# Kernel tuning notes

Hardware: AMD Instinct MI355X
Metric: run time of the kernel (lower is better)

## Reference

```python
import jax, jax.numpy as jnp
import numpy as np

N_NODES = 100000
N_EDGES = 1600000
D = 128


def setup_inputs() -> dict:
    key = jax.random.key(0)
    k1, k2, k3, k4 = jax.random.split(key, 4)
    x = jax.random.normal(k1, (N_NODES, D), dtype=jnp.float32)
    # scale weights by 1/sqrt(fan_in) (matches typical init, keeps exp(e) stable)
    W = jax.random.normal(k2, (D, D), dtype=jnp.float32) / np.sqrt(D)
    a = jax.random.normal(k3, (2 * D,), dtype=jnp.float32) / np.sqrt(2 * D)
    edge_index = jax.random.randint(k4, (2, N_EDGES), 0, N_NODES, dtype=jnp.int64)
    return {"x": x, "W": W, "a": a, "edge_index": edge_index}


def reference(x, W, a, edge_index):
    # x: [N, in], W: [out, in] (torch Linear layout), a: [2*out], edge_index: [2, E]
    N = x.shape[0]
    d_out = W.shape[0]
    h = x @ W.T                                   # [N, out]
    src = edge_index[0]
    tgt = edge_index[1]
    # a(cat([h_src, h_tgt])) == h_src @ a[:d] + h_tgt @ a[d:] — avoids [E, 2d] concat
    s_src = h @ a[:d_out]                         # [N]
    s_tgt = h @ a[d_out:]                         # [N]
    e = jax.nn.leaky_relu(s_src[src] + s_tgt[tgt], negative_slope=0.2)  # [E]
    att = jnp.exp(e)                              # [E]
    att_sum = jax.ops.segment_sum(att, tgt, num_segments=N)             # [N]
    att_norm = att / (att_sum[tgt] + 1e-8)        # [E] (dropout=0 / eval mode)
    h_prime = jax.ops.segment_sum(h[src] * att_norm[:, None], tgt, num_segments=N)  # [N, out]
    h_prime = h_prime + x                          # residual (in_features == out_features)
    return jax.nn.elu(h_prime)
```

## Files before the change

kernel.cpp:

```cpp
#include <hip/hip_runtime.h>
#include <hip/hip_bf16.h>

#define DD 128
#define CAP 56
#define NBPW 128
#define CHUNK 4096
#define LBIN 832

typedef _Float16 half8  __attribute__((ext_vector_type(8)));
typedef _Float16 half2t __attribute__((ext_vector_type(2)));
typedef float f32x4 __attribute__((ext_vector_type(4)));

__device__ __forceinline__ ushort h16bits(float f) {
    _Float16 h = (_Float16)f;
    return __builtin_bit_cast(ushort, h);
}
__device__ __forceinline__ half8 pack8h(float4 lo, float4 hi) {
    half8 r;
    r[0] = (_Float16)lo.x; r[1] = (_Float16)lo.y;
    r[2] = (_Float16)lo.z; r[3] = (_Float16)lo.w;
    r[4] = (_Float16)hi.x; r[5] = (_Float16)hi.y;
    r[6] = (_Float16)hi.z; r[7] = (_Float16)hi.w;
    return r;
}
__device__ __forceinline__ float fdot2u(uint pair, uint avp, float c) {
    return __builtin_amdgcn_fdot2(__builtin_bit_cast(half2t, pair),
                                  __builtin_bit_cast(half2t, avp), c, false);
}

__global__ __launch_bounds__(256) void prep_w(
    const float* __restrict__ W, _Float16* __restrict__ Wh) {
    int i = blockIdx.x * 256 + threadIdx.x;
    if (i < DD * DD) Wh[i] = (_Float16)W[i];
}

__global__ __launch_bounds__(256, 2) void mfma_gemm_kernel(
    const float* __restrict__ x, const _Float16* __restrict__ Wh,
    const float* __restrict__ a, ushort* __restrict__ h,
    float* __restrict__ ssrc, float* __restrict__ stgt, int N, int nTiles) {
    __shared__ ushort hl[4][16][136];
    const int wid = threadIdx.x >> 6;
    const int l   = threadIdx.x & 63;
    const int lr  = l & 15;
    const int lk  = l >> 4;

    half8 Bf[4][8];
    #pragma unroll
    for (int kt = 0; kt < 4; ++kt)
        #pragma unroll
        for (int n = 0; n < 8; ++n)
            Bf[kt][n] = *(const half8*)(Wh + (size_t)(n * 16 + lr) * DD + kt * 32 + lk * 8);
    float avs[8], avt[8];
    #pragma unroll
    for (int n = 0; n < 8; ++n) {
        avs[n] = a[n * 16 + lr];
        avt[n] = a[DD + n * 16 + lr];
    }

    for (int tile = blockIdx.x; tile < nTiles; tile += gridDim.x) {
        const int rowBase = tile * 64 + wid * 16;
        const int arow = rowBase + lr;
        f32x4 acc[8];
        #pragma unroll
        for (int n = 0; n < 8; ++n) acc[n] = (f32x4){0.f, 0.f, 0.f, 0.f};

        #pragma unroll
        for (int kt = 0; kt < 4; ++kt) {
            float4 x0, x1;
            if (arow < N) {
                const float* xp = x + (size_t)arow * DD + kt * 32 + lk * 8;
                x0 = *(const float4*)xp;
                x1 = *(const float4*)(xp + 4);
            } else {
                x0 = make_float4(0.f, 0.f, 0.f, 0.f);
                x1 = x0;
            }
            half8 A = pack8h(x0, x1);
            #pragma unroll
            for (int n = 0; n < 8; ++n)
                acc[n] = __builtin_amdgcn_mfma_f32_16x16x32_f16(A, Bf[kt][n], acc[n], 0, 0, 0);
        }

        float ps[4] = {0.f, 0.f, 0.f, 0.f}, pt[4] = {0.f, 0.f, 0.f, 0.f};
        #pragma unroll
        for (int n = 0; n < 8; ++n)
            #pragma unroll
            for (int r = 0; r < 4; ++r) {
                ps[r] = fmaf(acc[n][r], avs[n], ps[r]);
                pt[r] = fmaf(acc[n][r], avt[n], pt[r]);
            }
        #pragma unroll
        for (int r = 0; r < 4; ++r) {
            #pragma unroll
            for (int m = 8; m >= 1; m >>= 1) {
                ps[r] += __shfl_xor(ps[r], m);
                pt[r] += __shfl_xor(pt[r], m);
            }
        }
        if (lr == 0) {
            #pragma unroll
            for (int r = 0; r < 4; ++r) {
                int grow = rowBase + lk * 4 + r;
                if (grow < N) { ssrc[grow] = ps[r]; stgt[grow] = pt[r]; }
            }
        }

        __syncthreads();
        #pragma unroll
        for (int n = 0; n < 8; ++n)
            #pragma unroll
            for (int r = 0; r < 4; ++r)
                hl[wid][lk * 4 + r][n * 16 + lr] = h16bits(acc[n][r]);
        __syncthreads();
        if (arow < N) {
            uint4* dst = (uint4*)(h + (size_t)arow * DD + lk * 32);
            const uint4* s4 = (const uint4*)&hl[wid][lr][lk * 32];
            dst[0] = s4[0]; dst[1] = s4[1]; dst[2] = s4[2]; dst[3] = s4[3];
        }
    }
}

__global__ __launch_bounds__(256) void p1_count(
    const int* __restrict__ tgt, int* __restrict__ H, int E, int nbin, int nblk) {
    __shared__ int lh[LBIN];
    const int blk = blockIdx.x;
    for (int i = threadIdx.x; i < nbin; i += 256) lh[i] = 0;
    __syncthreads();
    const int base = blk * CHUNK;
    const int end = min(E, base + CHUNK);
    for (int e = base + threadIdx.x; e < end; e += 256)
        atomicAdd(&lh[tgt[e] >> 7], 1);
    __syncthreads();
    for (int i = threadIdx.x; i < nbin; i += 256) H[i * nblk + blk] = lh[i];
}

__global__ __launch_bounds__(256) void p2a_colscan(
    int* __restrict__ H, int* __restrict__ binTot, int nblk) {
    __shared__ int lds[256];
    const int o = blockIdx.x * nblk;
    const int t = threadIdx.x;
    int a0 = (2 * t     < nblk) ? H[o + 2 * t]     : 0;
    int a1 = (2 * t + 1 < nblk) ? H[o + 2 * t + 1] : 0;
    int s = a0 + a1;
    lds[t] = s;
    __syncthreads();
    int val = s;
    for (int off = 1; off < 256; off <<= 1) {
        int u = (t >= off) ? lds[t - off] : 0;
        __syncthreads();
        val += u;
        lds[t] = val;
        __syncthreads();
    }
    int excl = val - s;
    if (2 * t     < nblk) H[o + 2 * t]     = excl;
    if (2 * t + 1 < nblk) H[o + 2 * t + 1] = excl + a0;
    if (t == 255) binTot[blockIdx.x] = val;
}

__global__ __launch_bounds__(256) void p2b_binscan(
    const int* __restrict__ binTot, int* __restrict__ binOff, int nbin) {
    __shared__ int lds[256];
    const int t = threadIdx.x;
    int v[4];
    int s = 0;
    #pragma unroll
    for (int j = 0; j < 4; ++j) {
        int idx = t * 4 + j;
        v[j] = (idx < nbin) ? binTot[idx] : 0;
        s += v[j];
    }
    lds[t] = s;
    __syncthreads();
    int val = s;
    for (int off = 1; off < 256; off <<= 1) {
        int u = (t >= off) ? lds[t - off] : 0;
        __syncthreads();
        val += u;
        lds[t] = val;
        __syncthreads();
    }
    int excl = val - s;
    #pragma unroll
    for (int j = 0; j < 4; ++j) {
        int idx = t * 4 + j;
        if (idx < nbin) binOff[idx] = excl;
        excl += v[j];
    }
    if (t == 255) binOff[nbin] = val;
}

__global__ __launch_bounds__(256) void p3_partition(
    const int* __restrict__ src, const int* __restrict__ tgt,
    const int* __restrict__ H, const int* __restrict__ binOff,
    uint* __restrict__ ebuf, int E, int nbin, int nblk) {
    __shared__ int lcur[LBIN];
    const int blk = blockIdx.x;
    for (int i = threadIdx.x; i < nbin; i += 256) lcur[i] = 0;
    __syncthreads();
    const int base = blk * CHUNK;
    const int end = min(E, base + CHUNK);
    for (int e = base + threadIdx.x; e < end; e += 256) {
        int s = src[e], t = tgt[e];
        int tb = t >> 7;
        int r = atomicAdd(&lcur[tb], 1);
        int slot = binOff[tb] + H[tb * nblk + blk] + r;
        ebuf[slot] = ((uint)(t & 127) << 17) | (uint)s;
    }
}

__global__ __launch_bounds__(256) void p4_bucket(
    const uint* __restrict__ ebuf, const int* __restrict__ binOff,
    int* __restrict__ srcS, int* __restrict__ deg, int N) {
    __shared__ int cur[NBPW];
    const int bin = blockIdx.x;
    const int n0 = bin * NBPW;
    for (int i = threadIdx.x; i < NBPW; i += 256) cur[i] = 0;
    __syncthreads();
    const int beg = binOff[bin], end = binOff[bin + 1];
    for (int i = beg + threadIdx.x; i < end; i += 256) {
        uint v = ebuf[i];
        int tl = (int)(v >> 17);
        int s  = (int)(v & 0x1FFFFu);
        int pos = atomicAdd(&cur[tl], 1);
        if (pos < CAP) srcS[(size_t)(n0 + tl) * CAP + pos] = s;
    }
    __syncthreads();
    for (int i = threadIdx.x; i < NBPW; i += 256) {
        int node = n0 + i;
        if (node < N) deg[node] = cur[i];
    }
}

__global__ __launch_bounds__(256) void gather_acc_kernel(
    const int* __restrict__ srcS, const int* __restrict__ degA,
    const float* __restrict__ ssrc, const float* __restrict__ stgt,
    const ushort* __restrict__ h, const float* __restrict__ x,
    float* __restrict__ out, int N) {
    const int node = blockIdx.x * 4 + (threadIdx.x >> 6);
    if (node >= N) return;
    const int lane = threadIdx.x & 63;
    const int q = lane >> 4, l4 = lane & 15;

    int deg = degA[node];
    if (deg > CAP) deg = CAP;
    const size_t base = (size_t)node * CAP;

    int   sv = 0;
    float attv = 0.f;
    if (lane < deg) {
        sv = srcS[base + lane];
        float v = ssrc[sv] + stgt[node];
        v = v > 0.f ? v : 0.2f * v;
        attv = __expf(v);
    }
    float asum = attv;
    #pragma unroll
    for (int m = 32; m >= 1; m >>= 1) asum += __shfl_xor(asum, m);
    const float inv = 1.f / (asum + 1e-8f);
    const uint pv = ((uint)h16bits(attv) << 17) | (uint)sv;

    const int passes = (deg + 3) >> 2;
    float acc[8] = {0.f, 0.f, 0.f, 0.f, 0.f, 0.f, 0.f, 0.f};

    #define PAIR_STEP(pv0, pv1)                                                  \
    {                                                                            \
        int s0 = (int)((pv0) & 0x1FFFFu), s1 = (int)((pv1) & 0x1FFFFu);          \
        uint4 hv0 = *(const uint4*)(h + ((size_t)s0 << 7) + (l4 << 3));          \
        uint4 hv1 = *(const uint4*)(h + ((size_t)s1 << 7) + (l4 << 3));          \
        uint avp = ((pv0) >> 17) | (((pv1) >> 17) << 16);                        \
        uint p0, p1;                                                             \
        p0 = __builtin_amdgcn_perm(hv1.x, hv0.x, 0x05040100u);                   \
        p1 = __builtin_amdgcn_perm(hv1.x, hv0.x, 0x07060302u);                   \
        acc[0] = fdot2u(p0, avp, acc[0]); acc[1] = fdot2u(p1, avp, acc[1]);      \
        p0 = __builtin_amdgcn_perm(hv1.y, hv0.y, 0x05040100u);                   \
        p1 = __builtin_amdgcn_perm(hv1.y, hv0.y, 0x07060302u);                   \
        acc[2] = fdot2u(p0, avp, acc[2]); acc[3] = fdot2u(p1, avp, acc[3]);      \
        p0 = __builtin_amdgcn_perm(hv1.z, hv0.z, 0x05040100u);                   \
        p1 = __builtin_amdgcn_perm(hv1.z, hv0.z, 0x07060302u);                   \
        acc[4] = fdot2u(p0, avp, acc[4]); acc[5] = fdot2u(p1, avp, acc[5]);      \
        p0 = __builtin_amdgcn_perm(hv1.w, hv0.w, 0x05040100u);                   \
        p1 = __builtin_amdgcn_perm(hv1.w, hv0.w, 0x07060302u);                   \
        acc[6] = fdot2u(p0, avp, acc[6]); acc[7] = fdot2u(p1, avp, acc[7]);      \
    }

    int p = 0;
    for (; p + 4 <= passes; p += 4) {
        const int i0 = (p << 2) + q;
        uint a0 = (uint)__shfl((int)pv, i0);
        uint a1 = (uint)__shfl((int)pv, i0 + 4);
        uint a2 = (uint)__shfl((int)pv, i0 + 8);
        uint a3 = (uint)__shfl((int)pv, i0 + 12);
        PAIR_STEP(a0, a1);
        PAIR_STEP(a2, a3);
    }
    if (p + 2 <= passes) {
        const int i0 = (p << 2) + q;
        uint a0 = (uint)__shfl((int)pv, i0);
        uint a1 = (uint)__shfl((int)pv, i0 + 4);
        PAIR_STEP(a0, a1);
        p += 2;
    }
    if (p < passes) {
        const int i0 = (p << 2) + q;
        uint a0 = (uint)__shfl((int)pv, i0);
        int s0 = (int)(a0 & 0x1FFFFu);
        uint avp = a0 >> 17;
        uint4 hv0 = *(const uint4*)(h + ((size_t)s0 << 7) + (l4 << 3));
        acc[0] = fdot2u(hv0.x, avp, acc[0]); acc[1] = fdot2u(hv0.x >> 16, avp, acc[1]);
        acc[2] = fdot2u(hv0.y, avp, acc[2]); acc[3] = fdot2u(hv0.y >> 16, avp, acc[3]);
        acc[4] = fdot2u(hv0.z, avp, acc[4]); acc[5] = fdot2u(hv0.z >> 16, avp, acc[5]);
        acc[6] = fdot2u(hv0.w, avp, acc[6]); acc[7] = fdot2u(hv0.w >> 16, avp, acc[7]);
    }
    #undef PAIR_STEP

    #pragma unroll
    for (int j = 0; j < 8; ++j) {
        acc[j] += __shfl_xor(acc[j], 16);
        acc[j] += __shfl_xor(acc[j], 32);
    }

    if (q == 0) {
        const float4* xp = (const float4*)(x + (size_t)node * DD + l4 * 8);
        float4 x0 = xp[0], x1 = xp[1];
        float o[8];
        o[0] = fmaf(acc[0], inv, x0.x); o[1] = fmaf(acc[1], inv, x0.y);
        o[2] = fmaf(acc[2], inv, x0.z); o[3] = fmaf(acc[3], inv, x0.w);
        o[4] = fmaf(acc[4], inv, x1.x); o[5] = fmaf(acc[5], inv, x1.y);
        o[6] = fmaf(acc[6], inv, x1.z); o[7] = fmaf(acc[7], inv, x1.w);
        #pragma unroll
        for (int j = 0; j < 8; ++j) o[j] = o[j] > 0.f ? o[j] : expm1f(o[j]);
        float4* op = (float4*)(out + (size_t)node * DD + l4 * 8);
        op[0] = make_float4(o[0], o[1], o[2], o[3]);
        op[1] = make_float4(o[4], o[5], o[6], o[7]);
    }
}

extern "C" void kernel_launch(void* const* d_in, const int* in_sizes, int n_in,
                              void* d_out, int out_size, void* d_ws, size_t ws_size,
                              hipStream_t stream) {
    const float* x  = (const float*)d_in[0];
    const float* W  = (const float*)d_in[1];
    const float* a  = (const float*)d_in[2];
    const int*   ei = (const int*)d_in[3];

    const int N = in_sizes[0] / DD;
    const int E = in_sizes[3] / 2;
    const int* src = ei;
    const int* tgt = ei + E;

    float* out = (float*)d_out;

    const int nbin = (N + NBPW - 1) / NBPW;
    const int nblk = (E + CHUNK - 1) / CHUNK;

    char* w = (char*)d_ws;
    int*      srcS   = (int*)w;               w += (size_t)N * CAP * 4;
    ushort*   h      = (ushort*)w;            w += (size_t)N * DD * 2;
    float*    ssrc   = (float*)w;             w += (size_t)N * 4;
    float*    stgt   = (float*)w;             w += (size_t)N * 4;
    int*      deg    = (int*)w;               w += (size_t)N * 4;
    uint*     ebuf   = (uint*)w;              w += (size_t)E * 4;
    _Float16* Wh     = (_Float16*)w;          w += (size_t)DD * DD * 2;
    int*      H      = (int*)w;               w += (size_t)nbin * nblk * 4;
    int*      binTot = (int*)w;               w += (size_t)nbin * 4;
    int*      binOff = (int*)w;               w += (size_t)(nbin + 1) * 4;

    const int nTiles = (N + 63) / 64;

    prep_w<<<(DD * DD + 255) / 256, 256, 0, stream>>>(W, Wh);
    mfma_gemm_kernel<<<640, 256, 0, stream>>>(x, Wh, a, h, ssrc, stgt, N, nTiles);

    p1_count<<<nblk, 256, 0, stream>>>(tgt, H, E, nbin, nblk);
    p2a_colscan<<<nbin, 256, 0, stream>>>(H, binTot, nblk);
    p2b_binscan<<<1, 256, 0, stream>>>(binTot, binOff, nbin);
    p3_partition<<<nblk, 256, 0, stream>>>(src, tgt, H, binOff, ebuf, E, nbin, nblk);
    p4_bucket<<<nbin, 256, 0, stream>>>(ebuf, binOff, srcS, deg, N);

    gather_acc_kernel<<<(N + 3) / 4, 256, 0, stream>>>(srcS, deg, ssrc, stgt,
                                                       h, x, out, N);
}
```

Baseline: 164.3 us.

## Fuse histogram into GEMM, inline bin scan, half-wave per node gather

Merges the edge-count histogram into the GEMM kernel, which now launches one block per 64-row tile instead of a persistent grid. The bin-offset scan moves into every partition and bucket block, which removes two launches. The gather kernel now assigns a half-wave to each node, stages the packed (attention, src) pairs in LDS instead of using lane shuffles, and loads x early. The cost is redundant scan work in every block, and high-degree nodes now get fewer lanes each.

```diff
diff --git a/kernel.cpp b/kernel.cpp
--- a/kernel.cpp
+++ b/kernel.cpp
@@ -34,11 +34,14 @@
     if (i < DD * DD) Wh[i] = (_Float16)W[i];
 }
 
-__global__ __launch_bounds__(256, 2) void mfma_gemm_kernel(
+__global__ __launch_bounds__(256, 2) void gemm_hist_kernel(
     const float* __restrict__ x, const _Float16* __restrict__ Wh,
     const float* __restrict__ a, ushort* __restrict__ h,
-    float* __restrict__ ssrc, float* __restrict__ stgt, int N, int nTiles) {
+    float* __restrict__ ssrc, float* __restrict__ stgt,
+    const int* __restrict__ tgt, int* __restrict__ H,
+    int N, int E, int nbin, int nblk) {
     __shared__ ushort hl[4][16][136];
+    __shared__ int lh[LBIN];
     const int wid = threadIdx.x >> 6;
     const int l   = threadIdx.x & 63;
     const int lr  = l & 15;
@@ -57,81 +60,76 @@
         avt[n] = a[DD + n * 16 + lr];
     }
 
-    for (int tile = blockIdx.x; tile < nTiles; tile += gridDim.x) {
-        const int rowBase = tile * 64 + wid * 16;
-        const int arow = rowBase + lr;
-        f32x4 acc[8];
-        #pragma unroll
-        for (int n = 0; n < 8; ++n) acc[n] = (f32x4){0.f, 0.f, 0.f, 0.f};
-
-        #pragma unroll
-        for (int kt = 0; kt < 4; ++kt) {
-            float4 x0, x1;
-            if (arow < N) {
-                const float* xp = x + (size_t)arow * DD + kt * 32 + lk * 8;
-                x0 = *(const float4*)xp;
-                x1 = *(const float4*)(xp + 4);
-            } else {
-                x0 = make_float4(0.f, 0.f, 0.f, 0.f);
-                x1 = x0;
-            }
-            half8 A = pack8h(x0, x1);
-            #pragma unroll
-            for (int n = 0; n < 8; ++n)
-                acc[n] = __builtin_amdgcn_mfma_f32_16x16x32_f16(A, Bf[kt][n], acc[n], 0, 0, 0);
+    const int rowBase = blockIdx.x * 64 + wid * 16;
+    const int arow = rowBase + lr;
+    f32x4 acc[8];
+    #pragma unroll
+    for (int n = 0; n < 8; ++n) acc[n] = (f32x4){0.f, 0.f, 0.f, 0.f};
+
+    #pragma unroll
+    for (int kt = 0; kt < 4; ++kt) {
+        float4 x0, x1;
+        if (arow < N) {
+            const float* xp = x + (size_t)arow * DD + kt * 32 + lk * 8;
+            x0 = *(const float4*)xp;
+            x1 = *(const float4*)(xp + 4);
+        } else {
+            x0 = make_float4(0.f, 0.f, 0.f, 0.f);
+            x1 = x0;
         }
-
-        float ps[4] = {0.f, 0.f, 0.f, 0.f}, pt[4] = {0.f, 0.f, 0.f, 0.f};
+        half8 A = pack8h(x0, x1);
         #pragma unroll
         for (int n = 0; n < 8; ++n)
-            #pragma unroll
-            for (int r = 0; r < 4; ++r) {
-                ps[r] = fmaf(acc[n][r], avs[n], ps[r]);
-                pt[r] = fmaf(acc[n][r], avt[n], pt[r]);
-            }
+            acc[n] = __builtin_amdgcn_mfma_f32_16x16x32_f16(A, Bf[kt][n], acc[n], 0, 0, 0);
+    }
+
+    float ps[4] = {0.f, 0.f, 0.f, 0.f}, pt[4] = {0.f, 0.f, 0.f, 0.f};
+    #pragma unroll
+    for (int n = 0; n < 8; ++n)
         #pragma unroll
         for (int r = 0; r < 4; ++r) {
-            #pragma unroll
-            for (int m = 8; m >= 1; m >>= 1) {
-                ps[r] += __shfl_xor(ps[r], m);
-                pt[r] += __shfl_xor(pt[r], m);
-            }
+            ps[r] = fmaf(acc[n][r], avs[n], ps[r]);
+            pt[r] = fmaf(acc[n][r], avt[n], pt[r]);
         }
-        if (lr == 0) {
-            #pragma unroll
-            for (int r = 0; r < 4; ++r) {
-                int grow = rowBase + lk * 4 + r;
-                if (grow < N) { ssrc[grow] = ps[r]; stgt[grow] = pt[r]; }
-            }
+    #pragma unroll
+    for (int r = 0; r < 4; ++r) {
+        #pragma unroll
+        for (int m = 8; m >= 1; m >>= 1) {
+            ps[r] += __shfl_xor(ps[r], m);
+            pt[r] += __shfl_xor(pt[r], m);
         }
-
-        __syncthreads();
-        #pragma unroll
-        for (int n = 0; n < 8; ++n)
-            #pragma unroll
-            for (int r = 0; r < 4; ++r)
-                hl[wid][lk * 4 + r][n * 16 + lr] = h16bits(acc[n][r]);
-        __syncthreads();
-        if (arow < N) {
-            uint4* dst = (uint4*)(h + (size_t)arow * DD + lk * 32);
-            const uint4* s4 = (const uint4*)&hl[wid][lr][lk * 32];
-            dst[0] = s4[0]; dst[1] = s4[1]; dst[2] = s4[2]; dst[3] = s4[3];
+    }
+    if (lr == 0) {
+        #pragma unroll
+        for (int r = 0; r < 4; ++r) {
+            int grow = rowBase + lk * 4 + r;
+            if (grow < N) { ssrc[grow] = ps[r]; stgt[grow] = pt[r]; }
         }
     }
-}
-
-__global__ __launch_bounds__(256) void p1_count(
-    const int* __restrict__ tgt, int* __restrict__ H, int E, int nbin, int nblk) {
-    __shared__ int lh[LBIN];
-    const int blk = blockIdx.x;
-    for (int i = threadIdx.x; i < nbin; i += 256) lh[i] = 0;
-    __syncthreads();
-    const int base = blk * CHUNK;
-    const int end = min(E, base + CHUNK);
-    for (int e = base + threadIdx.x; e < end; e += 256)
-        atomicAdd(&lh[tgt[e] >> 7], 1);
-    __syncthreads();
-    for (int i = threadIdx.x; i < nbin; i += 256) H[i * nblk + blk] = lh[i];
+
+    #pragma unroll
+    for (int n = 0; n < 8; ++n)
+        #pragma unroll
+        for (int r = 0; r < 4; ++r)
+            hl[wid][lk * 4 + r][n * 16 + lr] = h16bits(acc[n][r]);
+    __syncthreads();
+    if (arow < N) {
+        uint4* dst = (uint4*)(h + (size_t)arow * DD + lk * 32);
+        const uint4* s4 = (const uint4*)&hl[wid][lr][lk * 32];
+        dst[0] = s4[0]; dst[1] = s4[1]; dst[2] = s4[2]; dst[3] = s4[3];
+    }
+
+    if (blockIdx.x < nblk) {
+        const int blk = blockIdx.x;
+        for (int i = threadIdx.x; i < nbin; i += 256) lh[i] = 0;
+        __syncthreads();
+        const int base = blk * CHUNK;
+        const int end = min(E, base + CHUNK);
+        for (int e = base + threadIdx.x; e < end; e += 256)
+            atomicAdd(&lh[tgt[e] >> 7], 1);
+        __syncthreads();
+        for (int i = threadIdx.x; i < nbin; i += 256) H[i * nblk + blk] = lh[i];
+    }
 }
 
 __global__ __launch_bounds__(256) void p2a_colscan(
@@ -158,8 +156,8 @@
     if (t == 255) binTot[blockIdx.x] = val;
 }
 
-__global__ __launch_bounds__(256) void p2b_binscan(
-    const int* __restrict__ binTot, int* __restrict__ binOff, int nbin) {
+__device__ __forceinline__ void scan_bins(const int* __restrict__ binTot,
+                                          int* __restrict__ binOffL, int nbin) {
     __shared__ int lds[256];
     const int t = threadIdx.x;
     int v[4];
@@ -184,17 +182,19 @@
     #pragma unroll
     for (int j = 0; j < 4; ++j) {
         int idx = t * 4 + j;
-        if (idx < nbin) binOff[idx] = excl;
+        if (idx < nbin) binOffL[idx] = excl;
         excl += v[j];
     }
-    if (t == 255) binOff[nbin] = val;
+    __syncthreads();
 }
 
 __global__ __launch_bounds__(256) void p3_partition(
     const int* __restrict__ src, const int* __restrict__ tgt,
-    const int* __restrict__ H, const int* __restrict__ binOff,
+    const int* __restrict__ H, const int* __restrict__ binTot,
     uint* __restrict__ ebuf, int E, int nbin, int nblk) {
+    __shared__ int binOffL[LBIN];
     __shared__ int lcur[LBIN];
+    scan_bins(binTot, binOffL, nbin);
     const int blk = blockIdx.x;
     for (int i = threadIdx.x; i < nbin; i += 256) lcur[i] = 0;
     __syncthreads();
@@ -204,20 +204,23 @@
         int s = src[e], t = tgt[e];
         int tb = t >> 7;
         int r = atomicAdd(&lcur[tb], 1);
-        int slot = binOff[tb] + H[tb * nblk + blk] + r;
+        int slot = binOffL[tb] + H[tb * nblk + blk] + r;
         ebuf[slot] = ((uint)(t & 127) << 17) | (uint)s;
     }
 }
 
 __global__ __launch_bounds__(256) void p4_bucket(
-    const uint* __restrict__ ebuf, const int* __restrict__ binOff,
-    int* __restrict__ srcS, int* __restrict__ deg, int N) {
+    const uint* __restrict__ ebuf, const int* __restrict__ binTot,
+    int* __restrict__ srcS, int* __restrict__ deg, int N, int nbin) {
+    __shared__ int binOffL[LBIN];
     __shared__ int cur[NBPW];
+    scan_bins(binTot, binOffL, nbin);
     const int bin = blockIdx.x;
     const int n0 = bin * NBPW;
     for (int i = threadIdx.x; i < NBPW; i += 256) cur[i] = 0;
     __syncthreads();
-    const int beg = binOff[bin], end = binOff[bin + 1];
+    const int beg = binOffL[bin];
+    const int end = beg + binTot[bin];
     for (int i = beg + threadIdx.x; i < end; i += 256) {
         uint v = ebuf[i];
         int tl = (int)(v >> 17);
@@ -237,30 +240,44 @@
     const float* __restrict__ ssrc, const float* __restrict__ stgt,
     const ushort* __restrict__ h, const float* __restrict__ x,
     float* __restrict__ out, int N) {
-    const int node = blockIdx.x * 4 + (threadIdx.x >> 6);
+    __shared__ uint lds_pv[8][64];
+    const int tid  = threadIdx.x;
+    const int wid  = tid >> 6, lane = tid & 63;
+    const int hw   = lane >> 5, hl = lane & 31;
+    const int g    = hl >> 4,   l4 = hl & 15;
+    const int nib  = (wid << 1) | hw;
+    const int node = blockIdx.x * 8 + nib;
     if (node >= N) return;
-    const int lane = threadIdx.x & 63;
-    const int q = lane >> 4, l4 = lane & 15;
-
+
+    const float4 xv = *(const float4*)(x + (size_t)node * DD + l4 * 8 + g * 4);
     int deg = degA[node];
     if (deg > CAP) deg = CAP;
+    const float st = stgt[node];
     const size_t base = (size_t)node * CAP;
 
-    int   sv = 0;
-    float attv = 0.f;
-    if (lane < deg) {
-        sv = srcS[base + lane];
-        float v = ssrc[sv] + stgt[node];
+    int sv0 = 0, sv1 = 0;
+    float att0 = 0.f, att1 = 0.f;
+    if (hl < deg) {
+        sv0 = srcS[base + hl];
+        float v = ssrc[sv0] + st;
         v = v > 0.f ? v : 0.2f * v;
-        attv = __expf(v);
-    }
-    float asum = attv;
-    #pragma unroll
-    for (int m = 32; m >= 1; m >>= 1) asum += __shfl_xor(asum, m);
+        att0 = __expf(v);
+    }
+    if (hl + 32 < deg) {
+        sv1 = srcS[base + hl + 32];
+        float v = ssrc[sv1] + st;
+        v = v > 0.f ? v : 0.2f * v;
+        att1 = __expf(v);
+    }
+    float asum = att0 + att1;
+    #pragma unroll
+    for (int m = 16; m >= 1; m >>= 1) asum += __shfl_xor(asum, m);
     const float inv = 1.f / (asum + 1e-8f);
-    const uint pv = ((uint)h16bits(attv) << 17) | (uint)sv;
-
-    const int passes = (deg + 3) >> 2;
+    lds_pv[nib][hl]      = ((uint)h16bits(att0) << 17) | (uint)sv0;
+    lds_pv[nib][hl + 32] = ((uint)h16bits(att1) << 17) | (uint)sv1;
+
+    const int passes = (deg + 1) >> 1;
+    const uint* pvrow = lds_pv[nib];
     float acc[8] = {0.f, 0.f, 0.f, 0.f, 0.f, 0.f, 0.f, 0.f};
 
     #define PAIR_STEP(pv0, pv1)                                                  \
@@ -286,24 +303,21 @@
 
     int p = 0;
     for (; p + 4 <= passes; p += 4) {
-        const int i0 = (p << 2) + q;
-        uint a0 = (uint)__shfl((int)pv, i0);
-        uint a1 = (uint)__shfl((int)pv, i0 + 4);
-        uint a2 = (uint)__shfl((int)pv, i0 + 8);
-        uint a3 = (uint)__shfl((int)pv, i0 + 12);
+        const int i0 = (p << 1) + g;
+        uint a0 = pvrow[i0], a1 = pvrow[i0 + 2];
+        uint a2 = pvrow[i0 + 4], a3 = pvrow[i0 + 6];
         PAIR_STEP(a0, a1);
         PAIR_STEP(a2, a3);
     }
     if (p + 2 <= passes) {
-        const int i0 = (p << 2) + q;
-        uint a0 = (uint)__shfl((int)pv, i0);
-        uint a1 = (uint)__shfl((int)pv, i0 + 4);
+        const int i0 = (p << 1) + g;
+        uint a0 = pvrow[i0], a1 = pvrow[i0 + 2];
         PAIR_STEP(a0, a1);
         p += 2;
     }
     if (p < passes) {
-        const int i0 = (p << 2) + q;
-        uint a0 = (uint)__shfl((int)pv, i0);
+        const int i0 = (p << 1) + g;
+        uint a0 = pvrow[i0];
         int s0 = (int)(a0 & 0x1FFFFu);
         uint avp = a0 >> 17;
         uint4 hv0 = *(const uint4*)(h + ((size_t)s0 << 7) + (l4 << 3));
@@ -315,25 +329,19 @@
     #undef PAIR_STEP
 
     #pragma unroll
-    for (int j = 0; j < 8; ++j) {
-        acc[j] += __shfl_xor(acc[j], 16);
-        acc[j] += __shfl_xor(acc[j], 32);
-    }
-
-    if (q == 0) {
-        const float4* xp = (const float4*)(x + (size_t)node * DD + l4 * 8);
-        float4 x0 = xp[0], x1 = xp[1];
-        float o[8];
-        o[0] = fmaf(acc[0], inv, x0.x); o[1] = fmaf(acc[1], inv, x0.y);
-        o[2] = fmaf(acc[2], inv, x0.z); o[3] = fmaf(acc[3], inv, x0.w);
-        o[4] = fmaf(acc[4], inv, x1.x); o[5] = fmaf(acc[5], inv, x1.y);
-        o[6] = fmaf(acc[6], inv, x1.z); o[7] = fmaf(acc[7], inv, x1.w);
-        #pragma unroll
-        for (int j = 0; j < 8; ++j) o[j] = o[j] > 0.f ? o[j] : expm1f(o[j]);
-        float4* op = (float4*)(out + (size_t)node * DD + l4 * 8);
-        op[0] = make_float4(o[0], o[1], o[2], o[3]);
-        op[1] = make_float4(o[4], o[5], o[6], o[7]);
-    }
+    for (int j = 0; j < 8; ++j) acc[j] += __shfl_xor(acc[j], 16);
+
+    float a0 = g ? acc[4] : acc[0];
+    float a1 = g ? acc[5] : acc[1];
+    float a2 = g ? acc[6] : acc[2];
+    float a3 = g ? acc[7] : acc[3];
+    float o0 = fmaf(a0, inv, xv.x), o1 = fmaf(a1, inv, xv.y);
+    float o2 = fmaf(a2, inv, xv.z), o3 = fmaf(a3, inv, xv.w);
+    o0 = o0 > 0.f ? o0 : expm1f(o0);
+    o1 = o1 > 0.f ? o1 : expm1f(o1);
+    o2 = o2 > 0.f ? o2 : expm1f(o2);
+    o3 = o3 > 0.f ? o3 : expm1f(o3);
+    *(float4*)(out + (size_t)node * DD + l4 * 8 + g * 4) = make_float4(o0, o1, o2, o3);
 }
 
 extern "C" void kernel_launch(void* const* d_in, const int* in_sizes, int n_in,
@@ -353,6 +361,7 @@
 
     const int nbin = (N + NBPW - 1) / NBPW;
     const int nblk = (E + CHUNK - 1) / CHUNK;
+    const int nTiles = (N + 63) / 64;
 
     char* w = (char*)d_ws;
     int*      srcS   = (int*)w;               w += (size_t)N * CAP * 4;
@@ -364,19 +373,13 @@
     _Float16* Wh     = (_Float16*)w;          w += (size_t)DD * DD * 2;
     int*      H      = (int*)w;               w += (size_t)nbin * nblk * 4;
     int*      binTot = (int*)w;               w += (size_t)nbin * 4;
-    int*      binOff = (int*)w;               w += (size_t)(nbin + 1) * 4;
-
-    const int nTiles = (N + 63) / 64;
 
     prep_w<<<(DD * DD + 255) / 256, 256, 0, stream>>>(W, Wh);
-    mfma_gemm_kernel<<<640, 256, 0, stream>>>(x, Wh, a, h, ssrc, stgt, N, nTiles);
-
-    p1_count<<<nblk, 256, 0, stream>>>(tgt, H, E, nbin, nblk);
+    gemm_hist_kernel<<<nTiles, 256, 0, stream>>>(x, Wh, a, h, ssrc, stgt,
+                                                 tgt, H, N, E, nbin, nblk);
     p2a_colscan<<<nbin, 256, 0, stream>>>(H, binTot, nblk);
-    p2b_binscan<<<1, 256, 0, stream>>>(binTot, binOff, nbin);
-    p3_partition<<<nblk, 256, 0, stream>>>(src, tgt, H, binOff, ebuf, E, nbin, nblk);
-    p4_bucket<<<nbin, 256, 0, stream>>>(ebuf, binOff, srcS, deg, N);
-
-    gather_acc_kernel<<<(N + 3) / 4, 256, 0, stream>>>(srcS, deg, ssrc, stgt,
+    p3_partition<<<nblk, 256, 0, stream>>>(src, tgt, H, binTot, ebuf, E, nbin, nblk);
+    p4_bucket<<<nbin, 256, 0, stream>>>(ebuf, binTot, srcS, deg, N, nbin);
+    gather_acc_kernel<<<(N + 7) / 8, 256, 0, stream>>>(srcS, deg, ssrc, stgt,
                                                        h, x, out, N);
 }
```

After: 162.7 us. About the same (-1.0%).
